# Optimization experiments

Measured on AMD Instinct MI355X. Metric: run time of the kernel, lower is better.

The kernel has to match this reference:

```python
import jax, jax.numpy as jnp
import numpy as np


def _conv2d(x, w, b):
    # 3x3 conv, stride 1, pad 1, NCHW
    y = jax.lax.conv_general_dilated(x, w, (1, 1), ((1, 1), (1, 1)),
                                     dimension_numbers=('NCHW', 'OIHW', 'NCHW'))
    return y + b[None, :, None, None]


def _up2(x):
    return jnp.repeat(jnp.repeat(x, 2, axis=2), 2, axis=3)


def _mdconv(x, w, b, ow, ob):
    # Modulated deformable conv v2 (mmcv semantics): 3x3, stride 1, pad 1,
    # dilation 1, deformable_groups=1. Offsets/mask predicted by conv_offset,
    # out = chunk3 -> (o1, o2, mask); offset = cat(o1, o2); mask = sigmoid(mask).
    B, Cin, H, W = x.shape
    off = _conv2d(x, ow, ob)                        # [B,27,H,W]
    o1, o2, m = jnp.split(off, 3, axis=1)
    offs = jnp.concatenate([o1, o2], axis=1)        # [B,18,H,W]
    dy, dx = offs[:, 0::2], offs[:, 1::2]           # [B,9,H,W] (dy,dx interleaved per kernel pt)
    mask = jax.nn.sigmoid(m)                        # [B,9,H,W]
    ky, kx = jnp.meshgrid(jnp.arange(3), jnp.arange(3), indexing='ij')
    # sampling positions: p0 + pn + offset (pad=1)
    py = jnp.arange(H, dtype=x.dtype)[None, None, :, None] - 1.0 + ky.reshape(1, 9, 1, 1) + dy
    px = jnp.arange(W, dtype=x.dtype)[None, None, None, :] - 1.0 + kx.reshape(1, 9, 1, 1) + dx
    y0 = jnp.floor(py); x0 = jnp.floor(px)
    wy1 = py - y0; wx1 = px - x0
    y0i = y0.astype(jnp.int32); x0i = x0.astype(jnp.int32)
    flat = x.reshape(B, Cin, H * W)

    def gather(yi, xi):
        valid = ((yi >= 0) & (yi < H) & (xi >= 0) & (xi < W)).astype(x.dtype)  # zero padding
        idx = jnp.clip(yi, 0, H - 1) * W + jnp.clip(xi, 0, W - 1)             # [B,9,H,W]
        g = jax.vmap(lambda f, i: f[:, i])(flat, idx)                          # [B,Cin,9,H,W]
        return g * valid[:, None]

    val = (gather(y0i, x0i) * ((1 - wy1) * (1 - wx1))[:, None]
           + gather(y0i, x0i + 1) * ((1 - wy1) * wx1)[:, None]
           + gather(y0i + 1, x0i) * (wy1 * (1 - wx1))[:, None]
           + gather(y0i + 1, x0i + 1) * (wy1 * wx1)[:, None])
    cols = val * mask[:, None]                      # [B,Cin,9,H,W]
    out = jnp.einsum('ock,bckhw->bohw', w.reshape(w.shape[0], Cin, 9), cols)
    return out + b[None, :, None, None]


def setup_inputs() -> dict:
    key = jax.random.key(0)
    ks = jax.random.split(key, 24)
    C = 256
    sizes = [(96, 96), (48, 48), (24, 24), (12, 12)]
    d = {}
    for i, (h, w) in enumerate(sizes):
        d[f'x{i}'] = jax.random.normal(ks[i], (2, C, h, w), dtype=jnp.float32)
    for i in range(4):
        d[f'w{i}'] = jax.random.normal(ks[4 + i], (C, C, 3, 3), dtype=jnp.float32) * 0.02
        d[f'b{i}'] = jax.random.normal(ks[8 + i], (C,), dtype=jnp.float32) * 0.02
    for i in range(1, 4):
        d[f'ow{i}'] = jax.random.normal(ks[12 + i], (27, C, 3, 3), dtype=jnp.float32) * 0.01
        d[f'ob{i}'] = jax.random.normal(ks[16 + i], (27,), dtype=jnp.float32) * 0.01
    return d


def reference(x0, x1, x2, x3, w0, w1, w2, w3, b0, b1, b2, b3,
              ow1, ow2, ow3, ob1, ob2, ob3):
    # tdm_convs[3] called with level=1 -> deform; the same-size nearest interpolate is identity
    t3 = _mdconv(x3, w3, b3, ow3, ob3)
    # i=3: tdm_convs[2](2, x2 + up(t3)) -> deform
    t2 = _mdconv(x2 + _up2(t3), w2, b2, ow2, ob2)
    # i=2: tdm_convs[1](1, x1 + up(t2)) -> deform
    t1 = _mdconv(x1 + _up2(t2), w1, b1, ow1, ob1)
    # i=1: tdm_convs[0](0, x0 + up(t1)) -> level 0 < start_level -> plain conv
    t0 = _conv2d(x0 + _up2(t1), w0, b0)
    return (t0, t1, t2, t3)
```

## Files before the change

kernel.cpp:

```cpp
#include <hip/hip_runtime.h>
#include <math.h>

__device__ __forceinline__ ushort f2bf(float f) {
    unsigned int u = __float_as_uint(f);
    u += 0x7FFFu + ((u >> 16) & 1u);
    return (ushort)(u >> 16);
}

typedef __attribute__((address_space(1))) const unsigned int guint;
typedef __attribute__((address_space(3))) unsigned int luint;
__device__ __forceinline__ void gload_lds16(const void* g, void* l) {
    __builtin_amdgcn_global_load_lds((guint*)g, (luint*)l, 16, 0, 0);
}

using bfrag = __attribute__((ext_vector_type(8))) short;
using f4    = __attribute__((ext_vector_type(4))) float;

__device__ __forceinline__ void bf8_to_f(uint4 v, float* o) {
    unsigned int u[4] = {v.x, v.y, v.z, v.w};
    #pragma unroll
    for (int i = 0; i < 4; ++i) {
        o[2 * i]     = __uint_as_float(u[i] << 16);
        o[2 * i + 1] = __uint_as_float(u[i] & 0xFFFF0000u);
    }
}

__device__ __forceinline__ void xs_body(void* smem,
    const float* __restrict__ x, const float* __restrict__ prev,
    ushort* __restrict__ xs, int H, int W, int bx, int by, int bz)
{
    ushort (*tile)[72] = (ushort(*)[72])smem;
    const int HW = H * W, W2 = W >> 1;
    int b = bz, c0 = by * 32, hw0 = bx * 64;
    const float* xb = x + ((size_t)b * 256 + c0) * HW;
    const float* pb = prev ? prev + ((size_t)b * 256 + c0) * (HW >> 2) : nullptr;

    int hwl = threadIdx.x & 63, cl0 = threadIdx.x >> 6;
    int hw = hw0 + hwl;
    bool ok = hw < HW;
    int hwc = ok ? hw : HW - 1;
    int h = hwc / W, w = hwc - h * W;
    int pidx = (h >> 1) * W2 + (w >> 1);
    #pragma unroll
    for (int p = 0; p < 8; ++p) {
        int cl = p * 4 + cl0;
        float v = 0.f;
        if (ok) {
            v = xb[(size_t)cl * HW + hw];
            if (pb) v += pb[(size_t)cl * (HW >> 2) + pidx];
        }
        tile[cl][hwl] = f2bf(v);
    }
    __syncthreads();
    int hwl2 = threadIdx.x >> 2, cc = (threadIdx.x & 3) * 8;
    int hw2 = hw0 + hwl2;
    if (hw2 < HW) {
        ushort vals[8];
        #pragma unroll
        for (int j = 0; j < 8; ++j) vals[j] = tile[cc + j][hwl2];
        *(uint4*)&xs[((size_t)b * HW + hw2) * 256 + c0 + cc] = *(uint4*)vals;
    }
}

struct ProArgs {
    const float* wsrc[7];
    ushort*      wdst[7];
    float*       outp[3];
    const float* bias[3];
    int          HW[3];
    float*       zbase;
    int          z4;
    const float* x3;
    ushort*      xs3;
};
__global__ __launch_bounds__(256) void prolog_kernel(ProArgs a) {
    __shared__ __align__(16) char smem[32 * 72 * 2];
    int y = blockIdx.y;
    if (y < 7) {
        int M = (y < 4) ? 256 : 27;
        int idx = blockIdx.x * 256 + threadIdx.x;
        if (idx < M * 288) {
            int m = idx / 288, rem = idx - m * 288;
            int r = rem >> 5, c8 = rem & 31;
            const float* s = a.wsrc[y] + ((size_t)(m * 256 + c8 * 8)) * 9 + r;
            ushort vals[8];
            #pragma unroll
            for (int j = 0; j < 8; ++j) vals[j] = f2bf(s[j * 9]);
            *(uint4*)&a.wdst[y][(size_t)m * 2304 + r * 256 + c8 * 8] = *(uint4*)vals;
        }
    } else if (y < 10) {
        int t = y - 7;
        int HW = a.HW[t];
        int i = blockIdx.x * 256 + threadIdx.x;
        if (i < 128 * HW) {
            int e = i << 2;
            int m = (e / HW) & 255;
            float v = a.bias[t][m];
            *(float4*)&a.outp[t][e] = float4{v, v, v, v};
        }
    } else if (y == 10) {
        int i = blockIdx.x * 256 + threadIdx.x;
        if (i < a.z4) ((float4*)a.zbase)[i] = float4{0.f, 0.f, 0.f, 0.f};
    } else {
        int vb = blockIdx.x;
        if (vb < 48)
            xs_body(smem, a.x3, nullptr, a.xs3, 12, 12, vb % 3, (vb / 3) & 7, vb / 24);
    }
}

__global__ __launch_bounds__(256) void xs_nhwc(
    const float* __restrict__ x, const float* __restrict__ prev,
    ushort* __restrict__ xs, int H, int W)
{
    __shared__ __align__(16) char smem[32 * 72 * 2];
    xs_body(smem, x, prev, xs, H, W, blockIdx.x, blockIdx.y, blockIdx.z);
}

__global__ __launch_bounds__(256) void off_mfma(
    const ushort* __restrict__ A, const ushort* __restrict__ xs,
    const ushort* __restrict__ zeros, float* __restrict__ offbuf,
    int N, int H, int W, int ktiles)
{
    __shared__ __align__(16) ushort As[2][32 * 32];
    __shared__ __align__(16) ushort Bs[2][64 * 32];
    const int b  = blockIdx.z;
    const int n0 = blockIdx.x * 64;
    const int kt0 = blockIdx.y * ktiles * 32;
    const int tid = threadIdx.x, lane = tid & 63, wv = tid >> 6;
    const ushort* xb = xs + (size_t)b * N * 256;

    int n = n0 + (tid >> 2); if (n >= N) n = N - 1;
    int h = n / W, w = n - h * W;
    int kcc = (tid & 3) * 8;

    auto stage = [&](int kt, int bi) {
        int r = kt >> 8, c0k = kt & 255;
        int ry = r / 3 - 1, rx = r - (r / 3) * 3 - 1;
        if (tid < 128) {
            int row = tid >> 2; if (row > 26) row = 26;
            gload_lds16(A + (size_t)row * 2304 + kt + kcc,
                        (char*)As[bi] + (size_t)(tid & ~63) * 16);
        }
        int ih = h + ry, iw = w + rx;
        const ushort* src = (ih >= 0 && ih < H && iw >= 0 && iw < W)
            ? xb + (((size_t)(ih * W + iw)) << 8) + c0k + kcc
            : zeros;
        gload_lds16(src, (char*)Bs[bi] + (size_t)(tid & ~63) * 16);
    };

    f4 acc[2] = {};
    stage(kt0, 0);
    for (int kk = 0; kk < ktiles; ++kk) {
        __syncthreads();
        if (kk + 1 < ktiles) stage(kt0 + (kk + 1) * 32, (kk + 1) & 1);
        const ushort* as = As[kk & 1];
        const ushort* bs = Bs[kk & 1];
        bfrag bf = *(const bfrag*)&bs[(wv * 16 + (lane & 15)) * 32 + (lane >> 4) * 8];
        bfrag a0 = *(const bfrag*)&as[(lane & 15) * 32 + (lane >> 4) * 8];
        bfrag a1 = *(const bfrag*)&as[(16 + (lane & 15)) * 32 + (lane >> 4) * 8];
        acc[0] = __builtin_amdgcn_mfma_f32_16x16x32_bf16(a0, bf, acc[0], 0, 0, 0);
        acc[1] = __builtin_amdgcn_mfma_f32_16x16x32_bf16(a1, bf, acc[1], 0, 0, 0);
    }

    int nn = n0 + wv * 16 + (lane & 15);
    if (nn < N) {
        #pragma unroll
        for (int mb = 0; mb < 2; ++mb)
            #pragma unroll
            for (int t = 0; t < 4; ++t) {
                int m = mb * 16 + (lane >> 4) * 4 + t;
                if (m < 27)
                    atomicAdd(&offbuf[((size_t)b * 27 + m) * N + nn], acc[mb][t]);
            }
    }
}

__global__ __launch_bounds__(256) void sampling_kernel(
    const ushort* __restrict__ xs, const float* __restrict__ off,
    const float* __restrict__ ob, ushort* __restrict__ cols,
    int H, int W)
{
    __shared__ float4 gw[32][9];
    __shared__ int4   go[32][9];
    const int HW = H * W;
    const int b = blockIdx.z;
    const int hw0 = blockIdx.x * 32;
    const int tid = threadIdx.x;
    const float* offb = off + (size_t)b * 27 * HW;
    const ushort* xb = xs + (size_t)b * HW * 256;

    for (int it = tid; it < 32 * 9; it += 256) {
        int hwl = it / 9, k = it - hwl * 9;
        int hw = hw0 + hwl; if (hw >= HW) hw = HW - 1;
        int h = hw / W, w = hw - h * W;
        float dy = offb[(size_t)(2 * k) * HW + hw] + ob[2 * k];
        float dx = offb[(size_t)(2 * k + 1) * HW + hw] + ob[2 * k + 1];
        float mv = offb[(size_t)(18 + k) * HW + hw] + ob[18 + k];
        float mk = 1.0f / (1.0f + __expf(-mv));
        float py = (float)h - 1.0f + (float)(k / 3) + dy;
        float px = (float)w - 1.0f + (float)(k % 3) + dx;
        float y0f = floorf(py), x0f = floorf(px);
        float wy = py - y0f, wx = px - x0f;
        int y0 = (int)y0f, x0i = (int)x0f;
        int y1 = y0 + 1, x1 = x0i + 1;
        bool vy0 = (y0 >= 0) & (y0 < H), vy1 = (y1 >= 0) & (y1 < H);
        bool vx0 = (x0i >= 0) & (x0i < W), vx1 = (x1 >= 0) & (x1 < W);
        float w00 = (1.f - wy) * (1.f - wx) * ((vy0 & vx0) ? mk : 0.f);
        float w01 = (1.f - wy) * wx        * ((vy0 & vx1) ? mk : 0.f);
        float w10 = wy * (1.f - wx)        * ((vy1 & vx0) ? mk : 0.f);
        float w11 = wy * wx                * ((vy1 & vx1) ? mk : 0.f);
        int cy0 = min(max(y0, 0), H - 1), cy1 = min(max(y1, 0), H - 1);
        int cx0 = min(max(x0i, 0), W - 1), cx1 = min(max(x1, 0), W - 1);
        gw[hwl][k] = float4{w00, w01, w10, w11};
        go[hwl][k] = int4{(cy0 * W + cx0) << 8, (cy0 * W + cx1) << 8,
                          (cy1 * W + cx0) << 8, (cy1 * W + cx1) << 8};
    }
    __syncthreads();

    int hwl = tid >> 3, cb = (tid & 7) * 32;
    int hw = hw0 + hwl;
    if (hw >= HW) return;
    ushort* colp = cols + ((size_t)b * HW + hw) * 2304 + cb;

    #pragma unroll
    for (int k = 0; k < 9; ++k) {
        float4 wv = gw[hwl][k];
        int4   ov = go[hwl][k];
        const ushort* p00 = xb + ov.x + cb;
        const ushort* p01 = xb + ov.y + cb;
        const ushort* p10 = xb + ov.z + cb;
        const ushort* p11 = xb + ov.w + cb;
        #pragma unroll
        for (int j = 0; j < 4; ++j) {
            float f00[8], f01[8], f10[8], f11[8];
            bf8_to_f(*(const uint4*)(p00 + 8 * j), f00);
            bf8_to_f(*(const uint4*)(p01 + 8 * j), f01);
            bf8_to_f(*(const uint4*)(p10 + 8 * j), f10);
            bf8_to_f(*(const uint4*)(p11 + 8 * j), f11);
            unsigned int pk[4];
            #pragma unroll
            for (int t = 0; t < 4; ++t) {
                float lo = f00[2 * t] * wv.x + f01[2 * t] * wv.y +
                           f10[2 * t] * wv.z + f11[2 * t] * wv.w;
                float hi = f00[2 * t + 1] * wv.x + f01[2 * t + 1] * wv.y +
                           f10[2 * t + 1] * wv.z + f11[2 * t + 1] * wv.w;
                pk[t] = (unsigned int)f2bf(lo) | ((unsigned int)f2bf(hi) << 16);
            }
            *(uint4*)(colp + k * 256 + 8 * j) = make_uint4(pk[0], pk[1], pk[2], pk[3]);
        }
    }
}

template<bool IMPLICIT, bool SPLITK>
__global__ __launch_bounds__(256) void mfma_gemm(
    const ushort* __restrict__ A, const float* __restrict__ bias,
    const ushort* __restrict__ Bt, const ushort* __restrict__ zeros,
    float* __restrict__ outp, int N, int H, int W, int kchunk)
{
    __shared__ __align__(16) ushort As[2][64 * 64];
    __shared__ __align__(16) ushort Bs[2][64 * 64];
    const int b  = blockIdx.z;
    const int m0 = (blockIdx.y & 3) * 64;
    const int kt0 = (blockIdx.y >> 2) * kchunk;
    const int n0 = blockIdx.x * 64;
    const int tid  = threadIdx.x;
    const int lane = tid & 63;
    const int wv   = tid >> 6;
    const int wm = wv & 1, wn = wv >> 1;

    const ushort* Bb = IMPLICIT ? Bt + (size_t)b * N * 256
                                : Bt + (size_t)b * (size_t)N * 2304;

    const int sc8 = ((tid & 7) ^ ((tid >> 3) & 7)) * 8;
    const int srow = tid >> 3;
    int bn[2], bh[2], bw[2];
    #pragma unroll
    for (int j = 0; j < 2; ++j) {
        int n = n0 + j * 32 + srow; if (n >= N) n = N - 1;
        bn[j] = n; bh[j] = n / W; bw[j] = n - bh[j] * W;
    }

    auto stage = [&](int kt, int bi) {
        #pragma unroll
        for (int i = 0; i < 2; ++i) {
            gload_lds16(A + (size_t)(m0 + i * 32 + srow) * 2304 + kt + sc8,
                        (char*)As[bi] + (size_t)(i * 256 + (tid & ~63)) * 16);
        }
        if (!IMPLICIT) {
            #pragma unroll
            for (int j = 0; j < 2; ++j)
                gload_lds16(Bb + (size_t)bn[j] * 2304 + kt + sc8,
                            (char*)Bs[bi] + (size_t)(j * 256 + (tid & ~63)) * 16);
        } else {
            int r = kt >> 8, c0k = kt & 255;
            int ry = r / 3 - 1, rx = r - (r / 3) * 3 - 1;
            #pragma unroll
            for (int j = 0; j < 2; ++j) {
                int ih = bh[j] + ry, iw = bw[j] + rx;
                const ushort* src = (ih >= 0 && ih < H && iw >= 0 && iw < W)
                    ? Bb + (((size_t)(ih * W + iw)) << 8) + c0k + sc8
                    : zeros;
                gload_lds16(src, (char*)Bs[bi] + (size_t)(j * 256 + (tid & ~63)) * 16);
            }
        }
    };

    const int fq = (lane >> 4);
    const int fv = (lane & 7);
    f4 acc[2][2] = {};

    const int nit = kchunk >> 6;
    stage(kt0, 0);
    for (int it = 0; it < nit; ++it) {
        __syncthreads();
        if (it + 1 < nit) stage(kt0 + (it + 1) * 64, (it + 1) & 1);
        const ushort* as = As[it & 1];
        const ushort* bs = Bs[it & 1];
        bfrag af[2][2], bf[2][2];
        #pragma unroll
        for (int kh = 0; kh < 2; ++kh) {
            int ch = ((kh * 4 + fq) ^ fv) * 8;
            #pragma unroll
            for (int i = 0; i < 2; ++i)
                af[kh][i] = *(const bfrag*)&as[(wm * 32 + i * 16 + (lane & 15)) * 64 + ch];
            #pragma unroll
            for (int j = 0; j < 2; ++j)
                bf[kh][j] = *(const bfrag*)&bs[(wn * 32 + j * 16 + (lane & 15)) * 64 + ch];
        }
        #pragma unroll
        for (int kh = 0; kh < 2; ++kh)
            #pragma unroll
            for (int i = 0; i < 2; ++i)
                #pragma unroll
                for (int j = 0; j < 2; ++j)
                    acc[i][j] = __builtin_amdgcn_mfma_f32_16x16x32_bf16(
                        af[kh][i], bf[kh][j], acc[i][j], 0, 0, 0);
    }

    const int mb = m0 + wm * 32, nb = n0 + wn * 32;
    #pragma unroll
    for (int i = 0; i < 2; ++i) {
        int mrow = mb + i * 16 + (lane >> 4) * 4;
        #pragma unroll
        for (int j = 0; j < 2; ++j) {
            int n = nb + j * 16 + (lane & 15);
            if (n < N) {
                #pragma unroll
                for (int t = 0; t < 4; ++t) {
                    int m = mrow + t;
                    if (SPLITK)
                        atomicAdd(&outp[((size_t)b * 256 + m) * N + n], acc[i][j][t]);
                    else
                        outp[((size_t)b * 256 + m) * N + n] = acc[i][j][t] + bias[m];
                }
            }
        }
    }
}

extern "C" void kernel_launch(void* const* d_in, const int* in_sizes, int n_in,
                              void* d_out, int out_size, void* d_ws, size_t ws_size,
                              hipStream_t stream)
{
    const float* x[4]   = {(const float*)d_in[0], (const float*)d_in[1],
                           (const float*)d_in[2], (const float*)d_in[3]};
    const float* wgt[4] = {(const float*)d_in[4], (const float*)d_in[6],
                           (const float*)d_in[8], (const float*)d_in[10]};
    const float* bia[4] = {(const float*)d_in[5], (const float*)d_in[7],
                           (const float*)d_in[9], (const float*)d_in[11]};
    const float* owt[4] = {nullptr, (const float*)d_in[12],
                           (const float*)d_in[14], (const float*)d_in[16]};
    const float* obv[4] = {nullptr, (const float*)d_in[13],
                           (const float*)d_in[15], (const float*)d_in[17]};

    const int B = 2;
    const int Hs[4] = {96, 48, 24, 12};
    const int HWs[4] = {96 * 96, 48 * 48, 24 * 24, 12 * 12};

    float* out = (float*)d_out;
    size_t outOff[4];
    outOff[0] = 0;
    outOff[1] = outOff[0] + (size_t)B * 256 * HWs[0];
    outOff[2] = outOff[1] + (size_t)B * 256 * HWs[1];
    outOff[3] = outOff[2] + (size_t)B * 256 * HWs[2];

    char* ws = (char*)d_ws;
    size_t off = 0;
    auto carve = [&](size_t bytes) { void* p = ws + off; off = (off + bytes + 255) & ~(size_t)255; return p; };
    ushort* wbf[4];
    ushort* owbf[4] = {nullptr, nullptr, nullptr, nullptr};
    for (int i = 0; i < 4; ++i) wbf[i] = (ushort*)carve((size_t)256 * 2304 * 2);
    for (int i = 1; i < 4; ++i) owbf[i] = (ushort*)carve((size_t)27 * 2304 * 2);
    ushort* cols = (ushort*)carve((size_t)B * HWs[1] * 2304 * 2);
    ushort* xsb[4];
    for (int i = 0; i < 4; ++i) xsb[i] = (ushort*)carve((size_t)B * 256 * HWs[i] * 2);
    int offElems = B * 27 * (HWs[1] + HWs[2] + HWs[3]);
    float* offbase = (float*)carve((size_t)offElems * 4 + 1024);
    ushort* zeros = (ushort*)(offbase + offElems);
    float* offbuf[4] = {nullptr,
                        offbase,
                        offbase + (size_t)B * 27 * HWs[1],
                        offbase + (size_t)B * 27 * (HWs[1] + HWs[2])};

    {
        ProArgs a;
        a.wsrc[0] = wgt[0]; a.wsrc[1] = wgt[1]; a.wsrc[2] = wgt[2]; a.wsrc[3] = wgt[3];
        a.wsrc[4] = owt[1]; a.wsrc[5] = owt[2]; a.wsrc[6] = owt[3];
        a.wdst[0] = wbf[0]; a.wdst[1] = wbf[1]; a.wdst[2] = wbf[2]; a.wdst[3] = wbf[3];
        a.wdst[4] = owbf[1]; a.wdst[5] = owbf[2]; a.wdst[6] = owbf[3];
        for (int i = 0; i < 3; ++i) {
            a.outp[i] = out + outOff[i + 1]; a.bias[i] = bia[i + 1]; a.HW[i] = HWs[i + 1];
        }
        a.zbase = offbase;
        a.z4 = (offElems * 4 + 1024) / 16;
        a.x3 = x[3];
        a.xs3 = xsb[3];
        dim3 grd(1152, 12);
        prolog_kernel<<<grd, 256, 0, stream>>>(a);
    }

    const int ktiles[4] = {0, 9, 6, 3};
    const int ksplit[4] = {1, 2, 6, 12};

    for (int lvl = 3; lvl >= 1; --lvl) {
        int H = Hs[lvl], W = H, HW = HWs[lvl];

        {
            dim3 grd((HW + 63) / 64, 72 / ktiles[lvl], B);
            off_mfma<<<grd, 256, 0, stream>>>(
                owbf[lvl], xsb[lvl], zeros, offbuf[lvl], HW, H, W, ktiles[lvl]);
        }
        {
            dim3 grd((HW + 31) / 32, 1, B);
            sampling_kernel<<<grd, 256, 0, stream>>>(
                xsb[lvl], offbuf[lvl], obv[lvl], cols, H, W);
        }
        {
            dim3 grd((HW + 63) / 64, 4 * ksplit[lvl], B);
            mfma_gemm<false, true><<<grd, 256, 0, stream>>>(
                wbf[lvl], bia[lvl], cols, zeros, out + outOff[lvl],
                HW, H, W, 2304 / ksplit[lvl]);
        }
        {
            int Hn = Hs[lvl - 1];
            dim3 grd((HWs[lvl - 1] + 63) / 64, 8, B);
            xs_nhwc<<<grd, 256, 0, stream>>>(
                x[lvl - 1], out + outOff[lvl], xsb[lvl - 1], Hn, Hn);
        }
    }

    {
        dim3 grd((HWs[0] + 63) / 64, 4, 2);
        mfma_gemm<true, false><<<grd, 256, 0, stream>>>(
            wbf[0], bia[0], xsb[0], zeros, out + outOff[0],
            HWs[0], Hs[0], Hs[0], 2304);
    }
}
```

Before: 290.2 us.

## Retile sampling kernel per-pixel-channel, add BM=128 tile for final conv, raise split-K

```diff
diff --git a/kernel.cpp b/kernel.cpp
--- a/kernel.cpp
+++ b/kernel.cpp
@@ -180,17 +180,17 @@
     const float* __restrict__ ob, ushort* __restrict__ cols,
     int H, int W)
 {
-    __shared__ float4 gw[32][9];
-    __shared__ int4   go[32][9];
+    __shared__ float4 gw[8][9];
+    __shared__ int4   go[8][9];
     const int HW = H * W;
     const int b = blockIdx.z;
-    const int hw0 = blockIdx.x * 32;
+    const int hw0 = blockIdx.x * 8;
     const int tid = threadIdx.x;
     const float* offb = off + (size_t)b * 27 * HW;
     const ushort* xb = xs + (size_t)b * HW * 256;
 
-    for (int it = tid; it < 32 * 9; it += 256) {
-        int hwl = it / 9, k = it - hwl * 9;
+    if (tid < 72) {
+        int hwl = tid / 9, k = tid - hwl * 9;
         int hw = hw0 + hwl; if (hw >= HW) hw = HW - 1;
         int h = hw / W, w = hw - h * W;
         float dy = offb[(size_t)(2 * k) * HW + hw] + ob[2 * k];
@@ -217,7 +217,7 @@
     }
     __syncthreads();
 
-    int hwl = tid >> 3, cb = (tid & 7) * 32;
+    int hwl = tid >> 5, cb = (tid & 31) * 8;
     int hw = hw0 + hwl;
     if (hw >= HW) return;
     ushort* colp = cols + ((size_t)b * HW + hw) * 2304 + cb;
@@ -226,42 +226,38 @@
     for (int k = 0; k < 9; ++k) {
         float4 wv = gw[hwl][k];
         int4   ov = go[hwl][k];
-        const ushort* p00 = xb + ov.x + cb;
-        const ushort* p01 = xb + ov.y + cb;
-        const ushort* p10 = xb + ov.z + cb;
-        const ushort* p11 = xb + ov.w + cb;
-        #pragma unroll
-        for (int j = 0; j < 4; ++j) {
-            float f00[8], f01[8], f10[8], f11[8];
-            bf8_to_f(*(const uint4*)(p00 + 8 * j), f00);
-            bf8_to_f(*(const uint4*)(p01 + 8 * j), f01);
-            bf8_to_f(*(const uint4*)(p10 + 8 * j), f10);
-            bf8_to_f(*(const uint4*)(p11 + 8 * j), f11);
-            unsigned int pk[4];
-            #pragma unroll
-            for (int t = 0; t < 4; ++t) {
-                float lo = f00[2 * t] * wv.x + f01[2 * t] * wv.y +
-                           f10[2 * t] * wv.z + f11[2 * t] * wv.w;
-                float hi = f00[2 * t + 1] * wv.x + f01[2 * t + 1] * wv.y +
-                           f10[2 * t + 1] * wv.z + f11[2 * t + 1] * wv.w;
-                pk[t] = (unsigned int)f2bf(lo) | ((unsigned int)f2bf(hi) << 16);
-            }
-            *(uint4*)(colp + k * 256 + 8 * j) = make_uint4(pk[0], pk[1], pk[2], pk[3]);
-        }
-    }
-}
-
-template<bool IMPLICIT, bool SPLITK>
+        float f00[8], f01[8], f10[8], f11[8];
+        bf8_to_f(*(const uint4*)(xb + ov.x + cb), f00);
+        bf8_to_f(*(const uint4*)(xb + ov.y + cb), f01);
+        bf8_to_f(*(const uint4*)(xb + ov.z + cb), f10);
+        bf8_to_f(*(const uint4*)(xb + ov.w + cb), f11);
+        unsigned int pk[4];
+        #pragma unroll
+        for (int t = 0; t < 4; ++t) {
+            float lo = f00[2 * t] * wv.x + f01[2 * t] * wv.y +
+                       f10[2 * t] * wv.z + f11[2 * t] * wv.w;
+            float hi = f00[2 * t + 1] * wv.x + f01[2 * t + 1] * wv.y +
+                       f10[2 * t + 1] * wv.z + f11[2 * t + 1] * wv.w;
+            pk[t] = (unsigned int)f2bf(lo) | ((unsigned int)f2bf(hi) << 16);
+        }
+        *(uint4*)(colp + k * 256) = make_uint4(pk[0], pk[1], pk[2], pk[3]);
+    }
+}
+
+template<bool IMPLICIT, bool SPLITK, int BM>
 __global__ __launch_bounds__(256) void mfma_gemm(
     const ushort* __restrict__ A, const float* __restrict__ bias,
     const ushort* __restrict__ Bt, const ushort* __restrict__ zeros,
     float* __restrict__ outp, int N, int H, int W, int kchunk)
 {
-    __shared__ __align__(16) ushort As[2][64 * 64];
+    constexpr int MT = 256 / BM;
+    constexpr int AL = BM / 32;
+    constexpr int AI = BM / 32;
+    __shared__ __align__(16) ushort As[2][BM * 64];
     __shared__ __align__(16) ushort Bs[2][64 * 64];
     const int b  = blockIdx.z;
-    const int m0 = (blockIdx.y & 3) * 64;
-    const int kt0 = (blockIdx.y >> 2) * kchunk;
+    const int m0 = (blockIdx.y % MT) * BM;
+    const int kt0 = (blockIdx.y / MT) * kchunk;
     const int n0 = blockIdx.x * 64;
     const int tid  = threadIdx.x;
     const int lane = tid & 63;
@@ -282,7 +278,7 @@
 
     auto stage = [&](int kt, int bi) {
         #pragma unroll
-        for (int i = 0; i < 2; ++i) {
+        for (int i = 0; i < AL; ++i) {
             gload_lds16(A + (size_t)(m0 + i * 32 + srow) * 2304 + kt + sc8,
                         (char*)As[bi] + (size_t)(i * 256 + (tid & ~63)) * 16);
         }
@@ -307,7 +303,7 @@
 
     const int fq = (lane >> 4);
     const int fv = (lane & 7);
-    f4 acc[2][2] = {};
+    f4 acc[AI][2] = {};
 
     const int nit = kchunk >> 6;
     stage(kt0, 0);
@@ -316,13 +312,13 @@
         if (it + 1 < nit) stage(kt0 + (it + 1) * 64, (it + 1) & 1);
         const ushort* as = As[it & 1];
         const ushort* bs = Bs[it & 1];
-        bfrag af[2][2], bf[2][2];
+        bfrag af[2][AI], bf[2][2];
         #pragma unroll
         for (int kh = 0; kh < 2; ++kh) {
             int ch = ((kh * 4 + fq) ^ fv) * 8;
             #pragma unroll
-            for (int i = 0; i < 2; ++i)
-                af[kh][i] = *(const bfrag*)&as[(wm * 32 + i * 16 + (lane & 15)) * 64 + ch];
+            for (int i = 0; i < AI; ++i)
+                af[kh][i] = *(const bfrag*)&as[(wm * (BM / 2) + i * 16 + (lane & 15)) * 64 + ch];
             #pragma unroll
             for (int j = 0; j < 2; ++j)
                 bf[kh][j] = *(const bfrag*)&bs[(wn * 32 + j * 16 + (lane & 15)) * 64 + ch];
@@ -330,16 +326,16 @@
         #pragma unroll
         for (int kh = 0; kh < 2; ++kh)
             #pragma unroll
-            for (int i = 0; i < 2; ++i)
+            for (int i = 0; i < AI; ++i)
                 #pragma unroll
                 for (int j = 0; j < 2; ++j)
                     acc[i][j] = __builtin_amdgcn_mfma_f32_16x16x32_bf16(
                         af[kh][i], bf[kh][j], acc[i][j], 0, 0, 0);
     }
 
-    const int mb = m0 + wm * 32, nb = n0 + wn * 32;
+    const int mb = m0 + wm * (BM / 2), nb = n0 + wn * 32;
     #pragma unroll
-    for (int i = 0; i < 2; ++i) {
+    for (int i = 0; i < AI; ++i) {
         int mrow = mb + i * 16 + (lane >> 4) * 4;
         #pragma unroll
         for (int j = 0; j < 2; ++j) {
@@ -420,7 +416,7 @@
     }
 
     const int ktiles[4] = {0, 9, 6, 3};
-    const int ksplit[4] = {1, 2, 6, 12};
+    const int ksplit[4] = {1, 4, 6, 12};
 
     for (int lvl = 3; lvl >= 1; --lvl) {
         int H = Hs[lvl], W = H, HW = HWs[lvl];
@@ -431,13 +427,13 @@
                 owbf[lvl], xsb[lvl], zeros, offbuf[lvl], HW, H, W, ktiles[lvl]);
         }
         {
-            dim3 grd((HW + 31) / 32, 1, B);
+            dim3 grd((HW + 7) / 8, 1, B);
             sampling_kernel<<<grd, 256, 0, stream>>>(
                 xsb[lvl], offbuf[lvl], obv[lvl], cols, H, W);
         }
         {
             dim3 grd((HW + 63) / 64, 4 * ksplit[lvl], B);
-            mfma_gemm<false, true><<<grd, 256, 0, stream>>>(
+            mfma_gemm<false, true, 64><<<grd, 256, 0, stream>>>(
                 wbf[lvl], bia[lvl], cols, zeros, out + outOff[lvl],
                 HW, H, W, 2304 / ksplit[lvl]);
         }
@@ -450,8 +446,8 @@
     }
 
     {
-        dim3 grd((HWs[0] + 63) / 64, 4, 2);
-        mfma_gemm<true, false><<<grd, 256, 0, stream>>>(
+        dim3 grd((HWs[0] + 63) / 64, 2, 2);
+        mfma_gemm<true, false, 128><<<grd, 256, 0, stream>>>(
             wbf[0], bia[0], xsb[0], zeros, out + outOff[0],
             HWs[0], Hs[0], Hs[0], 2304);
     }
```

New measurement: 256.8 us. 1.13x faster.
